# Optimization experiments

Hardware: AMD Instinct MI355X
Metric: run time of the kernel (lower is better)

Reference implementation:

```python
import jax, jax.numpy as jnp
import numpy as np

H = 8      # heads
D = 64     # dim_head
DIM = 512  # model dim (== H*D)
LN_EPS = 1e-5


def setup_inputs() -> dict:
    key = jax.random.key(0)
    ks = jax.random.split(key, 4)
    B, N = 8, 1024
    x = jax.random.normal(ks[0], (B, N, DIM), dtype=jnp.float32)
    # params (torch Linear y = x @ W^T; we store W already transposed as (in, out))
    w_qkv = jax.random.normal(ks[1], (DIM, 3 * H * D), dtype=jnp.float32) * (DIM ** -0.5)
    w_out = jax.random.normal(ks[2], (H * D, DIM), dtype=jnp.float32) * ((H * D) ** -0.5)
    b_out = jnp.zeros((DIM,), dtype=jnp.float32)
    ln_g = jnp.ones((DIM,), dtype=jnp.float32)
    ln_b = jnp.zeros((DIM,), dtype=jnp.float32)
    return {"x": x, "w_qkv": w_qkv, "w_out": w_out, "b_out": b_out,
            "ln_g": ln_g, "ln_b": ln_b}


def reference(x, w_qkv, w_out, b_out, ln_g, ln_b):
    b, n, _ = x.shape
    qkv = x @ w_qkv                                   # [b, n, 3*H*D]
    q, k, v = jnp.split(qkv, 3, axis=-1)              # each [b, n, H*D]

    def to_heads(t):                                  # 'b n (h d) -> (b h) n d'
        return t.reshape(b, n, H, D).transpose(0, 2, 1, 3).reshape(b * H, n, D)

    q = to_heads(q)
    k = to_heads(k)
    v = to_heads(v)

    # FAITHFUL to source: k.view(b*h, -1, n) is a row-major reshape, NOT a
    # transpose, and NO scale is applied (self.scale is unused in forward).
    k_r = k.reshape(b * H, D, n)                      # [(bh), D, n] reinterpreted
    dots = jnp.matmul(q, k_r)                          # [(bh), n, n]
    attn = jax.nn.softmax(dots, axis=-1)
    out = jnp.matmul(attn, v)                          # [(bh), n, D]

    # '(b h) n d -> b n (h d)'
    out = out.reshape(b, H, n, D).transpose(0, 2, 1, 3).reshape(b, n, H * D)
    out = out @ w_out + b_out                          # to_out Linear (dropout=0)

    mu = jnp.mean(out, axis=-1, keepdims=True)
    var = jnp.var(out, axis=-1, keepdims=True)
    out = (out - mu) * jax.lax.rsqrt(var + LN_EPS) * ln_g + ln_b
    return out + x
```

## Files before the change

kernel.cpp:

```cpp
#include <hip/hip_runtime.h>

typedef unsigned short u16;
typedef unsigned int u32;
typedef __attribute__((ext_vector_type(4))) float f32x4;
typedef __attribute__((ext_vector_type(8))) short s16x8;

__device__ __forceinline__ u16 bf16_rne(float f) {
    u32 u = __float_as_uint(f);
    u32 r = u + 0x7FFFu + ((u >> 16) & 1u);
    return (u16)(r >> 16);
}

__device__ __forceinline__ void gl_lds16(const void* g, void* l) {
    __builtin_amdgcn_global_load_lds(
        (const __attribute__((address_space(1))) u32*)g,
        (__attribute__((address_space(3))) u32*)l, 16, 0, 0);
}

#define MFMA16(a, b, c) __builtin_amdgcn_mfma_f32_16x16x32_bf16((a), (b), (c), 0, 0, 0)

__global__ __launch_bounds__(256) void k_convert(const float* __restrict__ in,
                                                 u16* __restrict__ out, int n4) {
    int i = blockIdx.x * 256 + threadIdx.x;
    if (i >= n4) return;
    f32x4 v = *(const f32x4*)(in + (size_t)i * 4);
    u32 lo = (u32)bf16_rne(v.x) | ((u32)bf16_rne(v.y) << 16);
    u32 hi = (u32)bf16_rne(v.z) | ((u32)bf16_rne(v.w) << 16);
    u32* p = (u32*)(out + (size_t)i * 4);
    p[0] = lo;
    p[1] = hi;
}

__global__ __launch_bounds__(256) void k_transpose_bf16(const float* __restrict__ in,
                                                        u16* __restrict__ out,
                                                        int R, int C) {
    __shared__ float tile[32][33];
    int bx = blockIdx.x * 32;
    int by = blockIdx.y * 32;
    int tx = threadIdx.x;
    int ty = threadIdx.y;
#pragma unroll
    for (int i = 0; i < 32; i += 8)
        tile[ty + i][tx] = in[(size_t)(by + ty + i) * C + bx + tx];
    __syncthreads();
#pragma unroll
    for (int i = 0; i < 32; i += 8)
        out[(size_t)(bx + ty + i) * R + by + tx] = bf16_rne(tile[tx][ty + i]);
}

__global__ __launch_bounds__(256) void k_qkv_gemm(
    const u16* __restrict__ xbf, const u16* __restrict__ wt,
    u16* __restrict__ qh, u16* __restrict__ kRT, u16* __restrict__ vT) {
    __shared__ __align__(16) u16 lA[2][128 * 64];
    __shared__ __align__(16) u16 lB[2][128 * 64];
    const int tid = threadIdx.x;
    const int lane = tid & 63, l15 = lane & 15, l4 = lane >> 4;
    const int wid = tid >> 6, wm = wid >> 1, wn = wid & 1;
    const int m0 = blockIdx.y * 128;
    const int c0 = blockIdx.x * 128;

    const char* gA = (const char*)xbf + (size_t)m0 * 1024;
    const char* gB = (const char*)wt + (size_t)c0 * 1024;
    const int srow = tid >> 3;
    const int scol = (tid & 7) * 16;

    const f32x4 z4 = {0.f, 0.f, 0.f, 0.f};
    f32x4 acc[4][4];
#pragma unroll
    for (int i = 0; i < 4; ++i)
#pragma unroll
        for (int j = 0; j < 4; ++j) acc[i][j] = z4;

    auto stage = [&](int buf, int kt) {
#pragma unroll
        for (int q = 0; q < 4; ++q) {
            int row = q * 32 + srow;
            int sc = scol ^ ((row & 7) << 4);
            gl_lds16(gA + (size_t)row * 1024 + kt * 128 + sc,
                     (char*)lA[buf] + q * 4096 + tid * 16);
            gl_lds16(gB + (size_t)row * 1024 + kt * 128 + sc,
                     (char*)lB[buf] + q * 4096 + tid * 16);
        }
    };

    stage(0, 0);
    __syncthreads();
    for (int kt = 0; kt < 8; ++kt) {
        int buf = kt & 1;
        if (kt < 7) stage(buf ^ 1, kt + 1);
        s16x8 af[4][2], bfr[4][2];
#pragma unroll
        for (int i = 0; i < 4; ++i)
#pragma unroll
            for (int k2 = 0; k2 < 2; ++k2) {
                int ra = wm * 64 + i * 16 + l15;
                int ca = (k2 * 64 + l4 * 16) ^ ((ra & 7) << 4);
                af[i][k2] = *(const s16x8*)((const char*)lA[buf] + ra * 128 + ca);
                int rb = wn * 64 + i * 16 + l15;
                int cb = (k2 * 64 + l4 * 16) ^ ((rb & 7) << 4);
                bfr[i][k2] = *(const s16x8*)((const char*)lB[buf] + rb * 128 + cb);
            }
#pragma unroll
        for (int i = 0; i < 4; ++i)
#pragma unroll
            for (int j = 0; j < 4; ++j)
#pragma unroll
                for (int k2 = 0; k2 < 2; ++k2)
                    acc[i][j] = MFMA16(af[i][k2], bfr[j][k2], acc[i][j]);
        __syncthreads();
    }

    char* ct = (char*)lA;
    const int which = c0 >> 9;
    const int hb = (c0 & 511) >> 6;
    const int b = m0 >> 10;
    const int n0 = m0 & 1023;
    const int i4 = (m0 >> 7) & 7;

    if (which != 2) {
#pragma unroll
        for (int i = 0; i < 4; ++i)
#pragma unroll
            for (int j = 0; j < 4; ++j) {
                int col = wn * 64 + j * 16 + l15;
#pragma unroll
                for (int r = 0; r < 4; ++r) {
                    int rr = wm * 64 + i * 16 + l4 * 4 + r;
                    *(u16*)(ct + rr * 256 + ((col * 2) ^ ((rr & 7) << 4))) =
                        bf16_rne(acc[i][j][r]);
                }
            }
    } else {
#pragma unroll
        for (int i = 0; i < 4; ++i)
#pragma unroll
            for (int j = 0; j < 4; ++j) {
                int col = wn * 64 + j * 16 + l15;
#pragma unroll
                for (int r = 0; r < 4; ++r) {
                    int rr = wm * 64 + i * 16 + l4 * 4 + r;
                    *(u16*)(ct + col * 256 + ((rr * 2) ^ ((col & 7) << 4))) =
                        bf16_rne(acc[i][j][r]);
                }
            }
    }
    __syncthreads();

    if (which == 0) {
#pragma unroll
        for (int p = 0; p < 8; ++p) {
            int cid = p * 256 + tid;
            int row = cid >> 4, sub = cid & 15;
            s16x8 v = *(const s16x8*)(ct + row * 256 + ((sub * 16) ^ ((row & 7) << 4)));
            int bh = b * 8 + hb + (sub >> 3);
            *(s16x8*)((char*)qh + ((size_t)bh * 1024 + n0 + row) * 128 +
                      (sub & 7) * 16) = v;
        }
    } else if (which == 1) {
#pragma unroll
        for (int p = 0; p < 8; ++p) {
            int cid = p * 256 + tid;
            int h = cid >> 10, jb = (cid >> 6) & 15, jd = cid & 63;
            int colb = ((h * 64 + jd) * 2) ^ ((jb & 7) << 4);
            s16x8 v;
#pragma unroll
            for (int ii = 0; ii < 8; ++ii)
                v[ii] = *(const short*)(ct + (jb + ii * 16) * 256 + colb);
            int bh = b * 8 + hb + h;
            *(s16x8*)((char*)kRT + (size_t)bh * 131072 + jb * 8192 + i4 * 1024 +
                      jd * 16) = v;
        }
    } else {
#pragma unroll
        for (int p = 0; p < 8; ++p) {
            int cid = p * 256 + tid;
            int cl = cid >> 4, nc = cid & 15;
            s16x8 v = *(const s16x8*)(ct + cl * 256 + ((nc * 16) ^ ((cl & 7) << 4)));
            int bh = b * 8 + hb + (cl >> 6);
            *(s16x8*)((char*)vT + ((size_t)bh * 64 + (cl & 63)) * 2048 + n0 * 2 +
                      nc * 16) = v;
        }
    }
}

__global__ __launch_bounds__(256) void k_attn(
    const u16* __restrict__ qh, const u16* __restrict__ kRT,
    const u16* __restrict__ vT, u16* __restrict__ attn_out) {
    __shared__ __align__(16) char smem[49152];
    char* qtile = smem;
    char* ktb = smem + 16384;
    char* vtb = smem + 32768;

    const int tid = threadIdx.x;
    const int lane = tid & 63, l15 = lane & 15, l4 = lane >> 4;
    const int wid = tid >> 6;
    const int bh = blockIdx.x, mt = blockIdx.y;

    const char* kb = (const char*)kRT + (size_t)bh * 131072;
    const char* vb = (const char*)vT + (size_t)bh * 64 * 2048;
    const int srow = tid >> 3, scol = (tid & 7) * 16;

    {
        const char* gq = (const char*)qh + ((size_t)bh * 1024 + mt * 128) * 128;
#pragma unroll
        for (int q = 0; q < 4; ++q) {
            int row = q * 32 + srow;
            int sc = scol ^ ((row & 7) << 4);
            gl_lds16(gq + (size_t)row * 128 + sc, qtile + q * 4096 + tid * 16);
        }
#pragma unroll
        for (int q = 0; q < 2; ++q) {
            int jd = q * 32 + srow;
            int i4s = (tid & 7) ^ (jd & 7);
            gl_lds16(kb + i4s * 1024 + jd * 16, ktb + q * 4096 + tid * 16);
            int sc = scol ^ ((jd & 7) << 4);
            gl_lds16(vb + (size_t)jd * 2048 + sc, vtb + q * 4096 + tid * 16);
        }
    }
    __syncthreads();

    s16x8 qf[2][2];
#pragma unroll
    for (int m2 = 0; m2 < 2; ++m2)
#pragma unroll
        for (int k2 = 0; k2 < 2; ++k2) {
            int row = wid * 32 + m2 * 16 + l15;
            int cq = (k2 * 64 + l4 * 16) ^ ((row & 7) << 4);
            qf[m2][k2] = *(const s16x8*)(qtile + row * 128 + cq);
        }
    __syncthreads();

    char* ptw = smem + wid * 4096;

    const f32x4 z4 = {0.f, 0.f, 0.f, 0.f};
    f32x4 o[2][4];
    f32x4 dacc[2];
#pragma unroll
    for (int m2 = 0; m2 < 2; ++m2) {
        dacc[m2] = z4;
#pragma unroll
        for (int j = 0; j < 4; ++j) o[m2][j] = z4;
    }
    const short one_bf = (short)0x3F80;
    const s16x8 ones = {one_bf, one_bf, one_bf, one_bf, one_bf, one_bf, one_bf, one_bf};
    const float LOG2E = 1.4426950408889634f;

#pragma unroll 2
    for (int jb = 0; jb < 16; ++jb) {
        const int buf = jb & 1;
        if (jb < 15) {
            int nb = jb + 1, bufn = buf ^ 1;
#pragma unroll
            for (int q = 0; q < 2; ++q) {
                int jd = q * 32 + srow;
                int i4s = (tid & 7) ^ (jd & 7);
                gl_lds16(kb + (size_t)nb * 8192 + i4s * 1024 + jd * 16,
                         ktb + bufn * 8192 + q * 4096 + tid * 16);
                int sc = scol ^ ((jd & 7) << 4);
                gl_lds16(vb + (size_t)jd * 2048 + nb * 128 + sc,
                         vtb + bufn * 8192 + q * 4096 + tid * 16);
            }
        }
        const char* kt = ktb + buf * 8192;
        const char* vt = vtb + buf * 8192;

        s16x8 bk[4][2];
#pragma unroll
        for (int n4 = 0; n4 < 4; ++n4)
#pragma unroll
            for (int k2 = 0; k2 < 2; ++k2) {
                int rn = n4 * 16 + l15;
                int cb = (k2 * 64 + l4 * 16) ^ ((rn & 7) << 4);
                bk[n4][k2] = *(const s16x8*)(kt + rn * 128 + cb);
            }
        f32x4 s[2][4];
        __builtin_amdgcn_s_setprio(1);
#pragma unroll
        for (int m2 = 0; m2 < 2; ++m2)
#pragma unroll
            for (int n4 = 0; n4 < 4; ++n4) {
                s[m2][n4] = z4;
#pragma unroll
                for (int k2 = 0; k2 < 2; ++k2)
                    s[m2][n4] = MFMA16(qf[m2][k2], bk[n4][k2], s[m2][n4]);
            }
        __builtin_amdgcn_s_setprio(0);

#pragma unroll
        for (int m2 = 0; m2 < 2; ++m2)
#pragma unroll
            for (int n4 = 0; n4 < 4; ++n4)
#pragma unroll
                for (int r = 0; r < 4; ++r) {
                    float e = exp2f(s[m2][n4][r] * LOG2E);
                    int row = m2 * 16 + l4 * 4 + r;
                    *(u16*)(ptw + row * 128 +
                            ((n4 * 32 + l15 * 2) ^ ((row & 7) << 4))) = bf16_rne(e);
                }

        s16x8 bv[4][2];
#pragma unroll
        for (int n4 = 0; n4 < 4; ++n4)
#pragma unroll
            for (int k2 = 0; k2 < 2; ++k2) {
                int rn = n4 * 16 + l15;
                int cb = (k2 * 64 + l4 * 16) ^ ((rn & 7) << 4);
                bv[n4][k2] = *(const s16x8*)(vt + rn * 128 + cb);
            }

        s16x8 pa[2][2];
#pragma unroll
        for (int m2 = 0; m2 < 2; ++m2)
#pragma unroll
            for (int k2 = 0; k2 < 2; ++k2) {
                int row = m2 * 16 + l15;
                pa[m2][k2] = *(const s16x8*)(ptw + row * 128 +
                                             ((k2 * 64 + l4 * 16) ^ ((row & 7) << 4)));
            }

        __builtin_amdgcn_s_setprio(1);
#pragma unroll
        for (int m2 = 0; m2 < 2; ++m2)
#pragma unroll
            for (int n4 = 0; n4 < 4; ++n4)
#pragma unroll
                for (int k2 = 0; k2 < 2; ++k2)
                    o[m2][n4] = MFMA16(pa[m2][k2], bv[n4][k2], o[m2][n4]);
#pragma unroll
        for (int m2 = 0; m2 < 2; ++m2)
#pragma unroll
            for (int k2 = 0; k2 < 2; ++k2)
                dacc[m2] = MFMA16(pa[m2][k2], ones, dacc[m2]);
        __builtin_amdgcn_s_setprio(0);

        if (jb < 15) __syncthreads();
    }

#pragma unroll
    for (int m2 = 0; m2 < 2; ++m2)
#pragma unroll
        for (int n4 = 0; n4 < 4; ++n4)
#pragma unroll
            for (int r = 0; r < 4; ++r) {
                float val = o[m2][n4][r] / dacc[m2][r];
                int rr = wid * 32 + m2 * 16 + l4 * 4 + r;
                int col = n4 * 16 + l15;
                *(u16*)(smem + rr * 128 + ((col * 2) ^ ((rr & 7) << 4))) =
                    bf16_rne(val);
            }
    __syncthreads();

    {
        char* dst = (char*)attn_out + ((size_t)(bh >> 3) * 1024 + mt * 128) * 1024 +
                    (bh & 7) * 128;
#pragma unroll
        for (int p = 0; p < 4; ++p) {
            int cid = p * 256 + tid;
            int row = cid >> 3, sub = cid & 7;
            s16x8 v = *(const s16x8*)(smem + row * 128 +
                                      ((sub * 16) ^ ((row & 7) << 4)));
            *(s16x8*)(dst + (size_t)row * 1024 + sub * 16) = v;
        }
    }
}

__global__ __launch_bounds__(256) void k_out_gemm(
    const u16* __restrict__ a, const u16* __restrict__ wt,
    const float* __restrict__ bias, float* __restrict__ proj) {
    __shared__ __align__(16) char smem[65536];
    u16* lA[2] = {(u16*)smem, (u16*)(smem + 16384)};
    u16* lB[2] = {(u16*)(smem + 32768), (u16*)(smem + 49152)};
    const int tid = threadIdx.x;
    const int lane = tid & 63, l15 = lane & 15, l4 = lane >> 4;
    const int wid = tid >> 6, wm = wid >> 1, wn = wid & 1;
    const int m0 = blockIdx.y * 128;
    const int c0 = blockIdx.x * 128;

    const char* gA = (const char*)a + (size_t)m0 * 1024;
    const char* gB = (const char*)wt + (size_t)c0 * 1024;
    const int srow = tid >> 3;
    const int scol = (tid & 7) * 16;

    const f32x4 z4 = {0.f, 0.f, 0.f, 0.f};
    f32x4 acc[4][4];
#pragma unroll
    for (int i = 0; i < 4; ++i)
#pragma unroll
        for (int j = 0; j < 4; ++j) acc[i][j] = z4;

    auto stage = [&](int buf, int kt) {
#pragma unroll
        for (int q = 0; q < 4; ++q) {
            int row = q * 32 + srow;
            int sc = scol ^ ((row & 7) << 4);
            gl_lds16(gA + (size_t)row * 1024 + kt * 128 + sc,
                     (char*)lA[buf] + q * 4096 + tid * 16);
            gl_lds16(gB + (size_t)row * 1024 + kt * 128 + sc,
                     (char*)lB[buf] + q * 4096 + tid * 16);
        }
    };

    stage(0, 0);
    __syncthreads();
    for (int kt = 0; kt < 8; ++kt) {
        int buf = kt & 1;
        if (kt < 7) stage(buf ^ 1, kt + 1);
        s16x8 af[4][2], bfr[4][2];
#pragma unroll
        for (int i = 0; i < 4; ++i)
#pragma unroll
            for (int k2 = 0; k2 < 2; ++k2) {
                int ra = wm * 64 + i * 16 + l15;
                int ca = (k2 * 64 + l4 * 16) ^ ((ra & 7) << 4);
                af[i][k2] = *(const s16x8*)((const char*)lA[buf] + ra * 128 + ca);
                int rb = wn * 64 + i * 16 + l15;
                int cb = (k2 * 64 + l4 * 16) ^ ((rb & 7) << 4);
                bfr[i][k2] = *(const s16x8*)((const char*)lB[buf] + rb * 128 + cb);
            }
#pragma unroll
        for (int i = 0; i < 4; ++i)
#pragma unroll
            for (int j = 0; j < 4; ++j)
#pragma unroll
                for (int k2 = 0; k2 < 2; ++k2)
                    acc[i][j] = MFMA16(af[i][k2], bfr[j][k2], acc[i][j]);
        __syncthreads();
    }

#pragma unroll
    for (int i = 0; i < 4; ++i)
#pragma unroll
        for (int j = 0; j < 4; ++j) {
            int col = wn * 64 + j * 16 + l15;
            float bo = bias[c0 + col];
#pragma unroll
            for (int r = 0; r < 4; ++r) {
                int rr = wm * 64 + i * 16 + l4 * 4 + r;
                *(float*)(smem + rr * 512 + ((col * 4) ^ ((rr & 7) << 4))) =
                    acc[i][j][r] + bo;
            }
        }
    __syncthreads();
#pragma unroll
    for (int p = 0; p < 16; ++p) {
        int cid = p * 256 + tid;
        int row = cid >> 5, sub = cid & 31;
        f32x4 v = *(const f32x4*)(smem + row * 512 + ((sub * 16) ^ ((row & 7) << 4)));
        *(f32x4*)((char*)proj + (size_t)(m0 + row) * 2048 + c0 * 4 + sub * 16) = v;
    }
}

__global__ __launch_bounds__(256) void k_ln(const float* __restrict__ proj,
                                            const float* __restrict__ x,
                                            const float* __restrict__ g,
                                            const float* __restrict__ bb,
                                            float* __restrict__ out) {
    const int lane = threadIdx.x & 63, wid = threadIdx.x >> 6;
    const int row = blockIdx.x * 4 + wid;
    const float* pr = proj + (size_t)row * 512;
    f32x4 v0 = *(const f32x4*)(pr + lane * 4);
    f32x4 v1 = *(const f32x4*)(pr + 256 + lane * 4);
    float s = v0.x + v0.y + v0.z + v0.w + v1.x + v1.y + v1.z + v1.w;
    float sq = v0.x * v0.x + v0.y * v0.y + v0.z * v0.z + v0.w * v0.w +
               v1.x * v1.x + v1.y * v1.y + v1.z * v1.z + v1.w * v1.w;
#pragma unroll
    for (int m = 1; m < 64; m <<= 1) {
        s += __shfl_xor(s, m);
        sq += __shfl_xor(sq, m);
    }
    float mu = s * (1.0f / 512.0f);
    float var = sq * (1.0f / 512.0f) - mu * mu;
    float rstd = rsqrtf(var + 1e-5f);

    const float* xr = x + (size_t)row * 512;
    f32x4 x0 = *(const f32x4*)(xr + lane * 4);
    f32x4 x1 = *(const f32x4*)(xr + 256 + lane * 4);
    f32x4 g0 = *(const f32x4*)(g + lane * 4);
    f32x4 g1 = *(const f32x4*)(g + 256 + lane * 4);
    f32x4 b0 = *(const f32x4*)(bb + lane * 4);
    f32x4 b1 = *(const f32x4*)(bb + 256 + lane * 4);
    f32x4 r0, r1;
#pragma unroll
    for (int u = 0; u < 4; ++u) {
        r0[u] = (v0[u] - mu) * rstd * g0[u] + b0[u] + x0[u];
        r1[u] = (v1[u] - mu) * rstd * g1[u] + b1[u] + x1[u];
    }
    float* orow = out + (size_t)row * 512;
    *(f32x4*)(orow + lane * 4) = r0;
    *(f32x4*)(orow + 256 + lane * 4) = r1;
}

extern "C" void kernel_launch(void* const* d_in, const int* in_sizes, int n_in,
                              void* d_out, int out_size, void* d_ws, size_t ws_size,
                              hipStream_t stream) {
    const float* x = (const float*)d_in[0];
    const float* w_qkv = (const float*)d_in[1];
    const float* w_out = (const float*)d_in[2];
    const float* b_out = (const float*)d_in[3];
    const float* ln_g = (const float*)d_in[4];
    const float* ln_b = (const float*)d_in[5];
    float* out = (float*)d_out;
    char* ws = (char*)d_ws;

    u16* xbf = (u16*)(ws + 0);
    u16* wqkvt = (u16*)(ws + 8388608);
    u16* woutt = (u16*)(ws + 9961472);
    u16* qh = (u16*)(ws + 10485760);
    u16* kRT = (u16*)(ws + 18874368);
    u16* vT = (u16*)(ws + 27262976);
    u16* aout = (u16*)(ws + 35651584);
    float* proj = (float*)(ws + 10485760);

    k_convert<<<4096, 256, 0, stream>>>(x, xbf, 1048576);
    k_transpose_bf16<<<dim3(48, 16), dim3(32, 8), 0, stream>>>(w_qkv, wqkvt, 512, 1536);
    k_transpose_bf16<<<dim3(16, 16), dim3(32, 8), 0, stream>>>(w_out, woutt, 512, 512);
    k_qkv_gemm<<<dim3(12, 64), 256, 0, stream>>>(xbf, wqkvt, qh, kRT, vT);
    k_attn<<<dim3(64, 8), 256, 0, stream>>>(qh, kRT, vT, aout);
    k_out_gemm<<<dim3(4, 64), 256, 0, stream>>>(aout, woutt, b_out, proj);
    k_ln<<<2048, 256, 0, stream>>>(proj, x, ln_g, ln_b, out);
}
```

Before: 93.52 us.

## Restructure attention kernel to 8 waves with transposed MFMA and scalar denominators

The attention kernel now launches 512 threads per block, with each wave owning 16 query rows instead of 32. The MFMAs are transposed (K/V as the A operand, Q/P as B) so each lane holds a contiguous run of probabilities, letting P be written to LDS as packed 8-byte stores via v_cvt_pk_bf16_f32. The softmax denominator is summed in scalars and reduced with shuffles rather than with an extra MFMA against a ones vector. The intent is more waves to hide latency and fewer LDS and conversion instructions, at the cost of more barrier participants and smaller per-wave MFMA reuse of the K/V fragments.

```diff
diff --git a/kernel.cpp b/kernel.cpp
--- a/kernel.cpp
+++ b/kernel.cpp
@@ -9,6 +9,12 @@
     u32 u = __float_as_uint(f);
     u32 r = u + 0x7FFFu + ((u >> 16) & 1u);
     return (u16)(r >> 16);
+}
+
+__device__ __forceinline__ u32 cvt_pk_bf16(float lo, float hi) {
+    u32 r;
+    asm("v_cvt_pk_bf16_f32 %0, %1, %2" : "=v"(r) : "v"(lo), "v"(hi));
+    return r;
 }
 
 __device__ __forceinline__ void gl_lds16(const void* g, void* l) {
@@ -183,7 +189,7 @@
     }
 }
 
-__global__ __launch_bounds__(256) void k_attn(
+__global__ __launch_bounds__(512) void k_attn(
     const u16* __restrict__ qh, const u16* __restrict__ kRT,
     const u16* __restrict__ vT, u16* __restrict__ attn_out) {
     __shared__ __align__(16) char smem[49152];
@@ -198,68 +204,52 @@
 
     const char* kb = (const char*)kRT + (size_t)bh * 131072;
     const char* vb = (const char*)vT + (size_t)bh * 64 * 2048;
-    const int srow = tid >> 3, scol = (tid & 7) * 16;
+    const int srow = tid >> 3;
+    const int scol = (tid & 7) * 16;
 
     {
         const char* gq = (const char*)qh + ((size_t)bh * 1024 + mt * 128) * 128;
 #pragma unroll
-        for (int q = 0; q < 4; ++q) {
-            int row = q * 32 + srow;
+        for (int q = 0; q < 2; ++q) {
+            int row = q * 64 + srow;
             int sc = scol ^ ((row & 7) << 4);
-            gl_lds16(gq + (size_t)row * 128 + sc, qtile + q * 4096 + tid * 16);
-        }
-#pragma unroll
-        for (int q = 0; q < 2; ++q) {
-            int jd = q * 32 + srow;
-            int i4s = (tid & 7) ^ (jd & 7);
-            gl_lds16(kb + i4s * 1024 + jd * 16, ktb + q * 4096 + tid * 16);
-            int sc = scol ^ ((jd & 7) << 4);
-            gl_lds16(vb + (size_t)jd * 2048 + sc, vtb + q * 4096 + tid * 16);
-        }
-    }
-    __syncthreads();
-
-    s16x8 qf[2][2];
-#pragma unroll
-    for (int m2 = 0; m2 < 2; ++m2)
-#pragma unroll
-        for (int k2 = 0; k2 < 2; ++k2) {
-            int row = wid * 32 + m2 * 16 + l15;
-            int cq = (k2 * 64 + l4 * 16) ^ ((row & 7) << 4);
-            qf[m2][k2] = *(const s16x8*)(qtile + row * 128 + cq);
-        }
-    __syncthreads();
-
-    char* ptw = smem + wid * 4096;
+            gl_lds16(gq + (size_t)row * 128 + sc, qtile + q * 8192 + tid * 16);
+        }
+        int i4s = (tid & 7) ^ (srow & 7);
+        gl_lds16(kb + i4s * 1024 + srow * 16, ktb + tid * 16);
+        int sc = scol ^ ((srow & 7) << 4);
+        gl_lds16(vb + (size_t)srow * 2048 + sc, vtb + tid * 16);
+    }
+    __syncthreads();
+
+    s16x8 qf[2];
+#pragma unroll
+    for (int k2 = 0; k2 < 2; ++k2) {
+        int row = wid * 16 + l15;
+        int cq = (k2 * 64 + l4 * 16) ^ ((row & 7) << 4);
+        qf[k2] = *(const s16x8*)(qtile + row * 128 + cq);
+    }
+    __syncthreads();
+
+    char* ptw = smem + wid * 2048;
 
     const f32x4 z4 = {0.f, 0.f, 0.f, 0.f};
-    f32x4 o[2][4];
-    f32x4 dacc[2];
-#pragma unroll
-    for (int m2 = 0; m2 < 2; ++m2) {
-        dacc[m2] = z4;
-#pragma unroll
-        for (int j = 0; j < 4; ++j) o[m2][j] = z4;
-    }
-    const short one_bf = (short)0x3F80;
-    const s16x8 ones = {one_bf, one_bf, one_bf, one_bf, one_bf, one_bf, one_bf, one_bf};
+    f32x4 o[4];
+    float den = 0.f;
+#pragma unroll
+    for (int d4 = 0; d4 < 4; ++d4) o[d4] = z4;
     const float LOG2E = 1.4426950408889634f;
 
-#pragma unroll 2
     for (int jb = 0; jb < 16; ++jb) {
         const int buf = jb & 1;
         if (jb < 15) {
             int nb = jb + 1, bufn = buf ^ 1;
-#pragma unroll
-            for (int q = 0; q < 2; ++q) {
-                int jd = q * 32 + srow;
-                int i4s = (tid & 7) ^ (jd & 7);
-                gl_lds16(kb + (size_t)nb * 8192 + i4s * 1024 + jd * 16,
-                         ktb + bufn * 8192 + q * 4096 + tid * 16);
-                int sc = scol ^ ((jd & 7) << 4);
-                gl_lds16(vb + (size_t)jd * 2048 + nb * 128 + sc,
-                         vtb + bufn * 8192 + q * 4096 + tid * 16);
-            }
+            int i4s = (tid & 7) ^ (srow & 7);
+            gl_lds16(kb + (size_t)nb * 8192 + i4s * 1024 + srow * 16,
+                     ktb + bufn * 8192 + tid * 16);
+            int sc = scol ^ ((srow & 7) << 4);
+            gl_lds16(vb + (size_t)srow * 2048 + nb * 128 + sc,
+                     vtb + bufn * 8192 + tid * 16);
         }
         const char* kt = ktb + buf * 8192;
         const char* vt = vtb + buf * 8192;
@@ -273,89 +263,81 @@
                 int cb = (k2 * 64 + l4 * 16) ^ ((rn & 7) << 4);
                 bk[n4][k2] = *(const s16x8*)(kt + rn * 128 + cb);
             }
-        f32x4 s[2][4];
+        f32x4 s[4];
         __builtin_amdgcn_s_setprio(1);
 #pragma unroll
-        for (int m2 = 0; m2 < 2; ++m2)
-#pragma unroll
-            for (int n4 = 0; n4 < 4; ++n4) {
-                s[m2][n4] = z4;
-#pragma unroll
-                for (int k2 = 0; k2 < 2; ++k2)
-                    s[m2][n4] = MFMA16(qf[m2][k2], bk[n4][k2], s[m2][n4]);
-            }
+        for (int n4 = 0; n4 < 4; ++n4) {
+            s[n4] = z4;
+#pragma unroll
+            for (int k2 = 0; k2 < 2; ++k2)
+                s[n4] = MFMA16(bk[n4][k2], qf[k2], s[n4]);
+        }
         __builtin_amdgcn_s_setprio(0);
 
 #pragma unroll
-        for (int m2 = 0; m2 < 2; ++m2)
-#pragma unroll
-            for (int n4 = 0; n4 < 4; ++n4)
-#pragma unroll
-                for (int r = 0; r < 4; ++r) {
-                    float e = exp2f(s[m2][n4][r] * LOG2E);
-                    int row = m2 * 16 + l4 * 4 + r;
-                    *(u16*)(ptw + row * 128 +
-                            ((n4 * 32 + l15 * 2) ^ ((row & 7) << 4))) = bf16_rne(e);
-                }
+        for (int n4 = 0; n4 < 4; ++n4) {
+            float e0 = exp2f(s[n4][0] * LOG2E);
+            float e1 = exp2f(s[n4][1] * LOG2E);
+            float e2 = exp2f(s[n4][2] * LOG2E);
+            float e3 = exp2f(s[n4][3] * LOG2E);
+            den += (e0 + e1) + (e2 + e3);
+            uint2 w;
+            w.x = cvt_pk_bf16(e0, e1);
+            w.y = cvt_pk_bf16(e2, e3);
+            *(uint2*)(ptw + l15 * 128 +
+                      ((n4 * 32 + l4 * 8) ^ ((l15 & 7) << 4))) = w;
+        }
 
         s16x8 bv[4][2];
 #pragma unroll
-        for (int n4 = 0; n4 < 4; ++n4)
+        for (int d4 = 0; d4 < 4; ++d4)
 #pragma unroll
             for (int k2 = 0; k2 < 2; ++k2) {
-                int rn = n4 * 16 + l15;
+                int rn = d4 * 16 + l15;
                 int cb = (k2 * 64 + l4 * 16) ^ ((rn & 7) << 4);
-                bv[n4][k2] = *(const s16x8*)(vt + rn * 128 + cb);
-            }
-
-        s16x8 pa[2][2];
-#pragma unroll
-        for (int m2 = 0; m2 < 2; ++m2)
-#pragma unroll
-            for (int k2 = 0; k2 < 2; ++k2) {
-                int row = m2 * 16 + l15;
-                pa[m2][k2] = *(const s16x8*)(ptw + row * 128 +
-                                             ((k2 * 64 + l4 * 16) ^ ((row & 7) << 4)));
-            }
+                bv[d4][k2] = *(const s16x8*)(vt + rn * 128 + cb);
+            }
+
+        s16x8 pa[2];
+#pragma unroll
+        for (int k2 = 0; k2 < 2; ++k2)
+            pa[k2] = *(const s16x8*)(ptw + l15 * 128 +
+                                     ((k2 * 64 + l4 * 16) ^ ((l15 & 7) << 4)));
 
         __builtin_amdgcn_s_setprio(1);
 #pragma unroll
-        for (int m2 = 0; m2 < 2; ++m2)
-#pragma unroll
-            for (int n4 = 0; n4 < 4; ++n4)
-#pragma unroll
-                for (int k2 = 0; k2 < 2; ++k2)
-                    o[m2][n4] = MFMA16(pa[m2][k2], bv[n4][k2], o[m2][n4]);
-#pragma unroll
-        for (int m2 = 0; m2 < 2; ++m2)
+        for (int d4 = 0; d4 < 4; ++d4)
 #pragma unroll
             for (int k2 = 0; k2 < 2; ++k2)
-                dacc[m2] = MFMA16(pa[m2][k2], ones, dacc[m2]);
+                o[d4] = MFMA16(bv[d4][k2], pa[k2], o[d4]);
         __builtin_amdgcn_s_setprio(0);
 
         if (jb < 15) __syncthreads();
     }
 
-#pragma unroll
-    for (int m2 = 0; m2 < 2; ++m2)
-#pragma unroll
-        for (int n4 = 0; n4 < 4; ++n4)
-#pragma unroll
-            for (int r = 0; r < 4; ++r) {
-                float val = o[m2][n4][r] / dacc[m2][r];
-                int rr = wid * 32 + m2 * 16 + l4 * 4 + r;
-                int col = n4 * 16 + l15;
-                *(u16*)(smem + rr * 128 + ((col * 2) ^ ((rr & 7) << 4))) =
-                    bf16_rne(val);
-            }
+    den += __shfl_xor(den, 16);
+    den += __shfl_xor(den, 32);
+    float inv = 1.0f / den;
+
+    {
+        int row = wid * 16 + l15;
+        char* ow = smem + row * 128;
+#pragma unroll
+        for (int d4 = 0; d4 < 4; ++d4) {
+            uint2 w;
+            w.x = cvt_pk_bf16(o[d4][0] * inv, o[d4][1] * inv);
+            w.y = cvt_pk_bf16(o[d4][2] * inv, o[d4][3] * inv);
+            *(uint2*)(ow + ((d4 * 32 + l4 * 8) ^ ((row & 7) << 4))) = w;
+        }
+    }
     __syncthreads();
 
     {
         char* dst = (char*)attn_out + ((size_t)(bh >> 3) * 1024 + mt * 128) * 1024 +
                     (bh & 7) * 128;
 #pragma unroll
-        for (int p = 0; p < 4; ++p) {
-            int cid = p * 256 + tid;
+        for (int p = 0; p < 2; ++p) {
+            int cid = p * 512 + tid;
             int row = cid >> 3, sub = cid & 7;
             s16x8 v = *(const s16x8*)(smem + row * 128 +
                                       ((sub * 16) ^ ((row & 7) << 4)));
@@ -515,7 +497,7 @@
     k_transpose_bf16<<<dim3(48, 16), dim3(32, 8), 0, stream>>>(w_qkv, wqkvt, 512, 1536);
     k_transpose_bf16<<<dim3(16, 16), dim3(32, 8), 0, stream>>>(w_out, woutt, 512, 512);
     k_qkv_gemm<<<dim3(12, 64), 256, 0, stream>>>(xbf, wqkvt, qh, kRT, vT);
-    k_attn<<<dim3(64, 8), 256, 0, stream>>>(qh, kRT, vT, aout);
+    k_attn<<<dim3(64, 8), 512, 0, stream>>>(qh, kRT, vT, aout);
     k_out_gemm<<<dim3(4, 64), 256, 0, stream>>>(aout, woutt, b_out, proj);
     k_ln<<<2048, 256, 0, stream>>>(proj, x, ln_g, ln_b, out);
 }
```

Measured after the change: 84.99 us. -9.1%, faster.
